# Kernel optimization log

Hardware: AMD Instinct MI355X
Metric: run time of the kernel (lower is better)

## Reference

```python
import jax, jax.numpy as jnp
import numpy as np

B, T, D, V, CD, NF = 2, 2048, 1024, 32000, 1024, 4
EPS_NORM = 1e-12
EPS_LN = 1e-5


def _gelu(x):
    return jax.nn.gelu(x, approximate=False)


def _l2norm(x):
    n = jnp.linalg.norm(x, axis=-1, keepdims=True)
    return x / jnp.maximum(n, EPS_NORM)


def setup_inputs() -> dict:
    key = jax.random.key(0)
    ks = jax.random.split(key, 24)
    s = 0.02
    inp = {
        "tokens": jax.random.randint(ks[0], (B, T), 0, V),
        "c_states": jax.random.normal(ks[1], (8, CD), dtype=jnp.float32),
        "embed": jax.random.normal(ks[2], (V, D), dtype=jnp.float32) * s,
        "pos_embed": jax.random.normal(ks[3], (T, D), dtype=jnp.float32) * s,
        # c_to_topo: Linear(c_dim,64) -> GELU -> Linear(64,2) -> Softplus (dead code in fwd, kept for completeness)
        "topo_W1": jax.random.normal(ks[4], (CD, 64), dtype=jnp.float32) * s,
        "topo_b1": jnp.zeros((64,), jnp.float32),
        "topo_W2": jax.random.normal(ks[5], (64, 2), dtype=jnp.float32) * s,
        "topo_b2": jnp.zeros((2,), jnp.float32),
        # c_to_thresh: Linear(c_dim,32) -> GELU -> Linear(32,NF) -> Sigmoid
        "thr_W1": jax.random.normal(ks[6], (CD, 32), dtype=jnp.float32) * s,
        "thr_b1": jnp.zeros((32,), jnp.float32),
        "thr_W2": jax.random.normal(ks[7], (32, NF), dtype=jnp.float32) * s,
        "thr_b2": jnp.zeros((NF,), jnp.float32),
        # simplex layers: NF x (Linear(2D,D) -> GELU -> Linear(D,D))
        "simp_W1": jax.random.normal(ks[8], (NF, 2 * D, D), dtype=jnp.float32) * s,
        "simp_b1": jnp.zeros((NF, D), jnp.float32),
        "simp_W2": jax.random.normal(ks[9], (NF, D, D), dtype=jnp.float32) * s,
        "simp_b2": jnp.zeros((NF, D), jnp.float32),
        # topo_integrate: Linear(D+2, 2D) -> GELU -> Linear(2D, D)
        "int_W1": jax.random.normal(ks[10], (D + 2, 2 * D), dtype=jnp.float32) * s,
        "int_b1": jnp.zeros((2 * D,), jnp.float32),
        "int_W2": jax.random.normal(ks[11], (2 * D, D), dtype=jnp.float32) * s,
        "int_b2": jnp.zeros((D,), jnp.float32),
        "ln_g": jnp.ones((D,), jnp.float32),
        "ln_b": jnp.zeros((D,), jnp.float32),
        "head_W": jax.random.normal(ks[12], (D, V), dtype=jnp.float32) * s,
    }
    return inp


def _forward(tokens, c_states, embed, pos_embed,
             topo_W1, topo_b1, topo_W2, topo_b2,
             thr_W1, thr_b1, thr_W2, thr_b2,
             simp_W1, simp_b1, simp_W2, simp_b2,
             int_W1, int_b1, int_W2, int_b2,
             ln_g, ln_b, head_W):
    b, t = tokens.shape
    x = embed[tokens] + pos_embed[jnp.arange(t)][None]          # [B,T,D]
    c_pooled = c_states.mean(axis=0)                            # [CD]
    thresholds = jax.nn.sigmoid(_gelu(c_pooled @ thr_W1 + thr_b1) @ thr_W2 + thr_b2)  # [NF]

    for level in range(NF):
        thresh = thresholds[level]
        x0 = x[0]                                               # [T,D] (module only uses batch elem 0)
        xn = _l2norm(x0)
        sim = xn @ xn.T                                         # [T,T]
        adj = jax.nn.sigmoid(10.0 * (sim - thresh))
        agg = adj @ x0                                          # dense message aggregation
        combined = jnp.concatenate([x0, agg], axis=-1)          # [T,2D]
        update = _gelu(combined @ simp_W1[level] + simp_b1[level]) @ simp_W2[level] + simp_b2[level]
        x = x + update[None] * 0.2                              # broadcast update across batch

    # approximate Betti numbers on detached embeddings
    xd = jax.lax.stop_gradient(x[0])
    xn = _l2norm(xd)
    sim = xn @ xn.T
    adj = jax.nn.sigmoid(10.0 * (sim - 0.5))
    degree = adj.sum(axis=-1)
    beta0 = (degree < 0.5).astype(jnp.float32).sum()
    n_edges = adj.sum() / 2.0
    beta1 = jax.nn.relu(n_edges - jnp.float32(t) + beta0 + 1.0)
    betti = jnp.stack([beta0, beta1])                           # [2]
    betti_exp = jnp.broadcast_to(betti[None, None, :], (b, t, 2))

    x = jnp.concatenate([x, betti_exp], axis=-1)                # [B,T,D+2]
    x = _gelu(x @ int_W1 + int_b1) @ int_W2 + int_b2            # [B,T,D]
    mu = x.mean(axis=-1, keepdims=True)
    var = x.var(axis=-1, keepdims=True)
    x = (x - mu) / jnp.sqrt(var + EPS_LN) * ln_g + ln_b
    return x @ head_W                                           # [B,T,V]


def reference(tokens, c_states, embed, pos_embed,
              topo_W1, topo_b1, topo_W2, topo_b2,
              thr_W1, thr_b1, thr_W2, thr_b2,
              simp_W1, simp_b1, simp_W2, simp_b2,
              int_W1, int_b1, int_W2, int_b2,
              ln_g, ln_b, head_W):
    return _forward(tokens, c_states, embed, pos_embed,
                    topo_W1, topo_b1, topo_W2, topo_b2,
                    thr_W1, thr_b1, thr_W2, thr_b2,
                    simp_W1, simp_b1, simp_W2, simp_b2,
                    int_W1, int_b1, int_W2, int_b2,
                    ln_g, ln_b, head_W)
```

## Files before the change

### kernel.cpp

```cpp
#include <hip/hip_runtime.h>

typedef __bf16 bf16;
using bf16x8 = __attribute__((ext_vector_type(8))) __bf16;
using bf16x4 = __attribute__((ext_vector_type(4))) __bf16;
using f32x4  = __attribute__((ext_vector_type(4))) float;

#define DEV __device__ __forceinline__
#define SCHED_FENCE() __builtin_amdgcn_sched_barrier(0)

DEV float gelu_f(float x){ return 0.5f*x*(1.0f+erff(x*0.7071067811865475f)); }
DEV float sigm_f(float x){ return 1.0f/(1.0f+expf(-x)); }

DEV void gload16(const bf16* g, bf16* l){
    __builtin_amdgcn_global_load_lds(
        (const __attribute__((address_space(1))) void*)g,
        (__attribute__((address_space(3))) void*)l, 16, 0, 0);
}

enum { EPI_ADJ=0, EPI_BF16=1, EPI_GELU_BIAS=2, EPI_XUPD=3, EPI_BIAS_F32=4, EPI_F32=5,
       EPI_XUPDB=6, EPI_XUPDT=7 };

template<int BM,int BN,int WM,int WN,int MINW,int EPI>
__global__ __launch_bounds__(WM*WN*64, MINW)
void gemm_p(const bf16* __restrict__ A, const bf16* __restrict__ B,
            int M, int N, int K, void* __restrict__ Cout, int ldc,
            const float* __restrict__ bias, const float* __restrict__ scal, int sidx,
            float* __restrict__ xu0, float* __restrict__ xu1, bf16* __restrict__ xbp)
{
    constexpr int THREADS = WM*WN*64;
    constexpr int MR = BM/WM/16, NR = BN/WN/16;
    constexpr int ATILE = BM*64, BTILE = BN*64;
    constexpr int RR = THREADS/8;
    constexpr int VM = (BM+BN)/RR;
    __shared__ bf16 sm[2*(ATILE+BTILE)];

    const int nbm = M/BM, nbn = N/BN;
    const int nwg = nbm*nbn;
    int wg = blockIdx.x;
    wg = (wg&7)*(nwg>>3) + (wg>>3);
    const int by = wg % nbm, bx = wg / nbm;
    const int tid = threadIdx.x, lane = tid&63, wid = tid>>6;
    const int wm = wid / WN, wn = wid % WN;
    const int fr = lane&15, fq = lane>>4;

    const bf16* Ab = A + (long)(by*BM + (tid>>3))*K + (((tid&7) ^ ((tid>>3)&7))<<3);
    const bf16* Bb = B + (long)(bx*BN + (tid>>3))*K + (((tid&7) ^ ((tid>>3)&7))<<3);

    auto STAGE = [&](int tt, int cb){
        bf16* d = sm + cb*(ATILE+BTILE) + wid*512;
        const long ko = (long)tt*64;
#pragma unroll
        for (int g=0; g<BM/RR; ++g)
            gload16(Ab + (long)g*RR*K + ko, d + g*RR*64);
#pragma unroll
        for (int g=0; g<BN/RR; ++g)
            gload16(Bb + (long)g*RR*K + ko, d + ATILE + g*RR*64);
    };

    f32x4 acc[MR][NR] = {};
    const int nt = K >> 6;

    STAGE(0,0);
    STAGE(1,1);

    for (int t=0; t<nt; ++t){
        const bf16* bufA = sm + (t&1)*(ATILE+BTILE);
        const bf16* bufB = bufA + ATILE;
        if (t+1<nt){
            if constexpr (VM==4)      asm volatile("s_waitcnt vmcnt(4)" ::: "memory");
            else if constexpr (VM==6) asm volatile("s_waitcnt vmcnt(6)" ::: "memory");
            else if constexpr (VM==8) asm volatile("s_waitcnt vmcnt(8)" ::: "memory");
            else                      asm volatile("s_waitcnt vmcnt(0)" ::: "memory");
        } else {
            asm volatile("s_waitcnt vmcnt(0)" ::: "memory");
        }
        __builtin_amdgcn_s_barrier();
        __builtin_amdgcn_sched_barrier(0);
#pragma unroll
        for (int ks=0; ks<2; ++ks){
            bf16x8 af[MR], bv[NR];
            const int ch = (((ks*4+fq) ^ (fr&7))<<3);
#pragma unroll
            for (int j=0;j<MR;++j)
                af[j] = *(const bf16x8*)&bufA[(wm*(MR*16) + j*16 + fr)*64 + ch];
#pragma unroll
            for (int j=0;j<NR;++j)
                bv[j] = *(const bf16x8*)&bufB[(wn*(NR*16) + j*16 + fr)*64 + ch];
            __builtin_amdgcn_s_setprio(1);
#pragma unroll
            for (int mi=0;mi<MR;++mi)
#pragma unroll
            for (int ni=0;ni<NR;++ni)
                acc[mi][ni] = __builtin_amdgcn_mfma_f32_16x16x32_bf16(
                    af[mi], bv[ni], acc[mi][ni], 0,0,0);
            __builtin_amdgcn_s_setprio(0);
        }
        asm volatile("s_waitcnt lgkmcnt(0)" ::: "memory");
        __builtin_amdgcn_s_barrier();
        if (t+2<nt) STAGE(t+2, t&1);
    }

    float thr = 0.f;
    if constexpr (EPI==EPI_ADJ) thr = scal[sidx];

#pragma unroll
    for (int mi=0;mi<MR;++mi){
#pragma unroll
        for (int ni=0;ni<NR;++ni){
            const int col = bx*BN + wn*(NR*16) + ni*16 + fr;
#pragma unroll
            for (int r=0;r<4;++r){
                const int row = by*BM + wm*(MR*16) + mi*16 + fq*4 + r;
                const float v = acc[mi][ni][r];
                const long ci = (long)row*ldc + col;
                if constexpr (EPI==EPI_ADJ)       ((bf16*)Cout)[ci] = (bf16)sigm_f(10.f*(v - thr));
                else if constexpr (EPI==EPI_BF16) ((bf16*)Cout)[ci] = (bf16)v;
                else if constexpr (EPI==EPI_GELU_BIAS) ((bf16*)Cout)[ci] = (bf16)gelu_f(v + bias[col]);
                else if constexpr (EPI==EPI_BIAS_F32)  ((float*)Cout)[ci] = v + bias[col];
                else if constexpr (EPI==EPI_F32)       ((float*)Cout)[ci] = v;
                else if constexpr (EPI==EPI_XUPD){
                    const float u = 0.2f*(v + bias[col]);
                    xu0[ci] += u;  xu1[ci] += u;
                }
                else if constexpr (EPI==EPI_XUPDB){
                    const float u = 0.2f*(v + bias[col]);
                    const float n0 = xu0[ci] + u, n1 = xu1[ci] + u;
                    xu0[ci] = n0;  xu1[ci] = n1;
                    xbp[ci] = (bf16)n0;
                    xbp[ci + (long)2048*1024] = (bf16)n1;
                }
                else if constexpr (EPI==EPI_XUPDT){
                    const float u = 0.2f*(v + bias[col]);
                    const float n0 = xu0[ci] + u, n1 = xu1[ci] + u;
                    xu0[ci] = n0;  xu1[ci] = n1;
                    ((bf16*)Cout)[(long)row*2048 + col] = (bf16)n0;
                    xbp[(long)col*2048 + row] = (bf16)n0;
                }
            }
        }
    }
}

template<int EPI>
__global__ __launch_bounds__(512, 2)
void gemm8(const bf16* __restrict__ A, const bf16* __restrict__ B,
           int M, int N, int K, void* __restrict__ Cout, int ldc,
           const float* __restrict__ bias)
{
    __shared__ bf16 sm[65536];
    const int nbm = M>>8;
    const int wg = blockIdx.x;
    const int by = wg % nbm, bx = wg / nbm;
    const int tid = threadIdx.x, lane = tid&63, wid = tid>>6;
    const int wm = wid>>2, wn = wid&3;
    const int fr = lane&15, fq = lane>>4;

    const bf16* Ag = A + (long)(by*256 + (tid>>3))*K + (((tid&7) ^ ((tid>>3)&7))<<3);
    const bf16* Bg = B + (long)(bx*256 + (tid>>3))*K + (((tid&7) ^ ((tid>>3)&7))<<3);

    auto SA = [&](int tt, int h){
        bf16* d = sm + (tt&1)*32768 + wid*512;
        const long ko = (long)tt*64;
        gload16(Ag + (long)(h*64)*K + ko,       d + h*4096);
        gload16(Ag + (long)(128+h*64)*K + ko,   d + 8192 + h*4096);
    };
    auto SB = [&](int tt, int h){
        bf16* d = sm + (tt&1)*32768 + 16384 + wid*512;
        const long ko = (long)tt*64;
#pragma unroll
        for (int g=0; g<2; ++g)
            gload16(Bg + (long)(h*2+g)*64*K + ko, d + (h*2+g)*4096);
    };

    f32x4 acc[8][4] = {};
    bf16x8 aCur[8], b0[4], b1[4];
    const int nt = K >> 6;

    SA(0,0); SB(0,0); SA(0,1); SB(0,1);
    SA(1,0); SB(1,0); SA(1,1);
    SCHED_FENCE();

    for (int t=0; t<nt; ++t){
        const bf16* bufA = sm + (t&1)*32768;
        const bf16* bufB = bufA + 16384;

        auto LDA = [&](int mh){
#pragma unroll
            for (int ks=0;ks<2;++ks){
                const int ch = (((ks*4+fq) ^ (fr&7))<<3);
#pragma unroll
                for (int j=0;j<4;++j)
                    aCur[ks*4+j] = *(const bf16x8*)&bufA[(wm*128 + mh*64 + j*16 + fr)*64 + ch];
            }
        };
        auto LDB = [&](int nh, bf16x8* dst){
#pragma unroll
            for (int ks=0;ks<2;++ks){
                const int ch = (((ks*4+fq) ^ (fr&7))<<3);
#pragma unroll
                for (int j=0;j<2;++j)
                    dst[ks*2+j] = *(const bf16x8*)&bufB[(wn*64 + nh*32 + j*16 + fr)*64 + ch];
            }
        };
        auto QMFMA = [&](int mh, int nh, bf16x8* bArr){
            __builtin_amdgcn_s_setprio(1);
#pragma unroll
            for (int ks=0;ks<2;++ks)
#pragma unroll
            for (int j=0;j<4;++j)
#pragma unroll
            for (int jj=0;jj<2;++jj)
                acc[mh*4+j][nh*2+jj] = __builtin_amdgcn_mfma_f32_16x16x32_bf16(
                    aCur[ks*4+j], bArr[ks*2+jj], acc[mh*4+j][nh*2+jj], 0,0,0);
            __builtin_amdgcn_s_setprio(0);
            SCHED_FENCE();
        };

        if (t+1<nt) asm volatile("s_waitcnt vmcnt(6)" ::: "memory");
        else        asm volatile("s_waitcnt vmcnt(0)" ::: "memory");
        __builtin_amdgcn_s_barrier();
        SCHED_FENCE();
        if (t+1<nt) SB(t+1,1);
        SCHED_FENCE();
        LDA(0); LDB(0, b0);
        asm volatile("s_waitcnt lgkmcnt(0)" ::: "memory");
        SCHED_FENCE();
        QMFMA(0,0,b0);
        __builtin_amdgcn_s_barrier();
        SCHED_FENCE();
        if (t+2<nt) SA(t+2,0);
        SCHED_FENCE();
        LDB(1, b1);
        asm volatile("s_waitcnt lgkmcnt(0)" ::: "memory");
        SCHED_FENCE();
        QMFMA(0,1,b1);
        __builtin_amdgcn_s_barrier();
        SCHED_FENCE();
        if (t+2<nt) SB(t+2,0);
        SCHED_FENCE();
        LDA(1);
        asm volatile("s_waitcnt lgkmcnt(0)" ::: "memory");
        SCHED_FENCE();
        QMFMA(1,1,b1);
        __builtin_amdgcn_s_barrier();
        SCHED_FENCE();
        if (t+2<nt) SA(t+2,1);
        SCHED_FENCE();
        QMFMA(1,0,b0);
    }

#pragma unroll
    for (int mi=0;mi<8;++mi){
#pragma unroll
        for (int ni=0;ni<4;++ni){
            const int col = bx*256 + wn*64 + ni*16 + fr;
#pragma unroll
            for (int r=0;r<4;++r){
                const int row = by*256 + wm*128 + mi*16 + fq*4 + r;
                const float v = acc[mi][ni][r];
                const long ci = (long)row*ldc + col;
                if constexpr (EPI==EPI_F32)            ((float*)Cout)[ci] = v;
                else if constexpr (EPI==EPI_BIAS_F32)  ((float*)Cout)[ci] = v + bias[col];
                else                                   ((bf16*)Cout)[ci] = (bf16)v;
            }
        }
    }
}

__global__ void prep_kernel(const float* __restrict__ cs,
                            const float* __restrict__ W1, const float* __restrict__ b1,
                            const float* __restrict__ W2, const float* __restrict__ b2,
                            float* __restrict__ thrs)
{
    __shared__ float cp[1024];
    __shared__ float part[8][32];
    __shared__ float h[32];
    const int tid = threadIdx.x;
    for (int j = tid; j < 1024; j += 256){
        float s = 0.f;
#pragma unroll
        for (int r = 0; r < 8; r++) s += cs[r*1024 + j];
        cp[j] = s * 0.125f;
    }
    __syncthreads();
    const int t = tid & 31, g = tid >> 5;
    float p = 0.f;
    for (int j = g*128; j < g*128+128; j++) p += cp[j] * W1[j*32 + t];
    part[g][t] = p;
    __syncthreads();
    if (tid < 32){
        float s = b1[tid];
#pragma unroll
        for (int q=0;q<8;q++) s += part[q][tid];
        h[tid] = gelu_f(s);
    }
    __syncthreads();
    if (tid < 4){
        float z = b2[tid];
        for (int k=0;k<32;k++) z += h[k]*W2[k*4 + tid];
        thrs[tid] = sigm_f(z);
    }
    if (tid == 4) thrs[4] = 0.5f;
}

__global__ void embed_kernel(const int* __restrict__ tok, const float* __restrict__ emb,
                             const float* __restrict__ pos, float* __restrict__ x)
{
    const long i = (long)blockIdx.x*256 + threadIdx.x;
    const int  d4 = i & 255;
    const long bt = i >> 8;
    const int  t  = (int)(bt & 2047);
    const int  token = tok[bt];
    f32x4 e = *(const f32x4*)(emb + (long)token*1024 + d4*4);
    f32x4 p = *(const f32x4*)(pos + (long)t*1024 + d4*4);
    *(f32x4*)(x + i*4) = e + p;
}

__global__ void transpose_f2b(const float* __restrict__ in, int ldin, long istr,
                              bf16* __restrict__ out, int ldout, long ostr,
                              int R, int C)
{
    __shared__ float tile[32][33];
    const int nbx = C >> 5, nby = R >> 5;
    const int per = nbx*nby;
    const int l  = blockIdx.x / per;
    const int rm = blockIdx.x % per;
    const int bx = rm % nbx, by = rm / nbx;
    const float* inl = in + (long)l*istr;
    bf16* outl = out + (long)l*ostr;
    const int tx = threadIdx.x & 31, ty = threadIdx.x >> 5;
#pragma unroll
    for (int i=0;i<32;i+=8)
        tile[ty+i][tx] = inl[(long)(by*32+ty+i)*ldin + bx*32+tx];
    __syncthreads();
#pragma unroll
    for (int i=0;i<32;i+=8)
        outl[(long)(bx*32+ty+i)*ldout + by*32+tx] = (bf16)tile[tx][ty+i];
}

__global__ void rownorm_kernel(const float* __restrict__ x, bf16* __restrict__ xn,
                               bf16* __restrict__ x0b, int ld0)
{
    const long t = blockIdx.x; const int tid = threadIdx.x;
    f32x4 v = *(const f32x4*)(x + t*1024 + tid*4);
    float s = v.x*v.x + v.y*v.y + v.z*v.z + v.w*v.w;
#pragma unroll
    for (int o=32;o>0;o>>=1) s += __shfl_down(s, o);
    __shared__ float red[4];
    if ((tid&63)==0) red[tid>>6] = s;
    __syncthreads();
    const float tot = red[0]+red[1]+red[2]+red[3];
    const float inv = 1.0f / fmaxf(sqrtf(tot), 1e-12f);
    bf16x4 a;
    a[0]=(bf16)(v.x*inv); a[1]=(bf16)(v.y*inv); a[2]=(bf16)(v.z*inv); a[3]=(bf16)(v.w*inv);
    *(bf16x4*)(xn + t*1024 + tid*4) = a;
    if (x0b){
        bf16x4 b;
        b[0]=(bf16)v.x; b[1]=(bf16)v.y; b[2]=(bf16)v.z; b[3]=(bf16)v.w;
        *(bf16x4*)(x0b + t*ld0 + tid*4) = b;
    }
}

__global__ void degree_kernel(const bf16* __restrict__ adj, float* __restrict__ deg)
{
    const long t = blockIdx.x; const int tid = threadIdx.x;
    bf16x8 v = *(const bf16x8*)(adj + t*2048 + tid*8);
    float s = 0.f;
#pragma unroll
    for (int j=0;j<8;j++) s += (float)v[j];
#pragma unroll
    for (int o=32;o>0;o>>=1) s += __shfl_down(s, o);
    __shared__ float red[4];
    if ((tid&63)==0) red[tid>>6] = s;
    __syncthreads();
    if (tid==0) deg[t] = red[0]+red[1]+red[2]+red[3];
}

__global__ void betti_kernel(const float* __restrict__ deg, float* __restrict__ betti)
{
    const int tid = threadIdx.x;
    float s = 0.f, c = 0.f;
#pragma unroll
    for (int i=0;i<8;i++){
        const float d = deg[tid*8 + i];
        s += d;  c += (d < 0.5f) ? 1.f : 0.f;
    }
#pragma unroll
    for (int o=32;o>0;o>>=1){ s += __shfl_down(s,o); c += __shfl_down(c,o); }
    __shared__ float ss[4], cc[4];
    if ((tid&63)==0){ ss[tid>>6]=s; cc[tid>>6]=c; }
    __syncthreads();
    if (tid==0){
        const float S = ss[0]+ss[1]+ss[2]+ss[3];
        const float C = cc[0]+cc[1]+cc[2]+cc[3];
        const float ne = 0.5f*S;
        const float b1 = ne - 2048.f + C + 1.f;
        betti[0] = C;
        betti[1] = b1 > 0.f ? b1 : 0.f;
    }
}

__global__ void b1eff_kernel(const float* __restrict__ ib1, const float* __restrict__ iW1,
                             const float* __restrict__ betti, float* __restrict__ out)
{
    const int j = blockIdx.x*256 + threadIdx.x;
    out[j] = ib1[j] + betti[0]*iW1[(long)1024*2048 + j] + betti[1]*iW1[(long)1025*2048 + j];
}

__global__ void ln_kernel(const float* __restrict__ y, const float* __restrict__ g,
                          const float* __restrict__ b, bf16* __restrict__ out)
{
    const long t = blockIdx.x; const int tid = threadIdx.x;
    f32x4 v = *(const f32x4*)(y + t*1024 + tid*4);
    float s  = v.x+v.y+v.z+v.w;
    float s2 = v.x*v.x+v.y*v.y+v.z*v.z+v.w*v.w;
#pragma unroll
    for (int o=32;o>0;o>>=1){ s += __shfl_down(s,o); s2 += __shfl_down(s2,o); }
    __shared__ float ss[4], qq[4];
    if ((tid&63)==0){ ss[tid>>6]=s; qq[tid>>6]=s2; }
    __syncthreads();
    const float S = ss[0]+ss[1]+ss[2]+ss[3], Q = qq[0]+qq[1]+qq[2]+qq[3];
    const float mu  = S * (1.f/1024.f);
    const float var = Q * (1.f/1024.f) - mu*mu;
    const float inv = rsqrtf(var + 1e-5f);
    f32x4 gv = *(const f32x4*)(g + tid*4);
    f32x4 bv = *(const f32x4*)(b + tid*4);
    bf16x4 o;
    o[0] = (bf16)((v.x - mu)*inv*gv.x + bv.x);
    o[1] = (bf16)((v.y - mu)*inv*gv.y + bv.y);
    o[2] = (bf16)((v.z - mu)*inv*gv.z + bv.z);
    o[3] = (bf16)((v.w - mu)*inv*gv.w + bv.w);
    *(bf16x4*)(out + t*1024 + tid*4) = o;
}

extern "C" void kernel_launch(void* const* d_in, const int* in_sizes, int n_in,
                              void* d_out, int out_size, void* d_ws, size_t ws_size,
                              hipStream_t stream)
{
    const int*   tokens = (const int*)  d_in[0];
    const float* cstate = (const float*)d_in[1];
    const float* embedW = (const float*)d_in[2];
    const float* posW   = (const float*)d_in[3];
    const float* thrW1  = (const float*)d_in[8];
    const float* thrb1  = (const float*)d_in[9];
    const float* thrW2  = (const float*)d_in[10];
    const float* thrb2  = (const float*)d_in[11];
    const float* simpW1 = (const float*)d_in[12];
    const float* simpb1 = (const float*)d_in[13];
    const float* simpW2 = (const float*)d_in[14];
    const float* simpb2 = (const float*)d_in[15];
    const float* intW1  = (const float*)d_in[16];
    const float* intb1  = (const float*)d_in[17];
    const float* intW2  = (const float*)d_in[18];
    const float* intb2  = (const float*)d_in[19];
    const float* lng    = (const float*)d_in[20];
    const float* lnb    = (const float*)d_in[21];
    const float* headW  = (const float*)d_in[22];
    float* out = (float*)d_out;

    size_t off = 0;
    auto carve = [&](size_t bytes) -> void* {
        void* p = (char*)d_ws + off;
        off += (bytes + 255) & ~(size_t)255;
        return p;
    };
    float* x_f32   = (float*)carve(16777216);
    bf16*  xn      = (bf16*) carve(4194304);
    bf16*  x0T     = (bf16*) carve(4194304);
    bf16*  comb    = (bf16*) carve(8388608);
    bf16*  adj     = (bf16*) carve(8388608);
    bf16*  h1      = (bf16*) carve(4194304);
    bf16*  xb      = (bf16*) carve(8388608);
    bf16*  w1T     = (bf16*) carve(16777216);
    bf16*  w2T     = (bf16*) carve(8388608);
    bf16*  i1T     = (bf16*) carve(4194304);
    bf16*  i2T     = (bf16*) carve(4194304);
    bf16*  hT      = (bf16*) carve(65536000);
    float* degree  = (float*)carve(8192);
    float* b1eff   = (float*)carve(8192);
    float* thrs    = (float*)carve(64);
    float* betti   = (float*)carve(64);
    bf16*  h2  = comb;
    float* yv  = x_f32;
    bf16*  xln = xn;

    const dim3 blk(256);
    const dim3 blk512(512);

    prep_kernel<<<1, blk, 0, stream>>>(cstate, thrW1, thrb1, thrW2, thrb2, thrs);
    embed_kernel<<<4096, blk, 0, stream>>>(tokens, embedW, posW, x_f32);

    transpose_f2b<<<4*(1024/32)*(2048/32), blk, 0, stream>>>(
        simpW1, 1024, (long)2048*1024, w1T, 2048, (long)1024*2048, 2048, 1024);
    transpose_f2b<<<4*(1024/32)*(1024/32), blk, 0, stream>>>(
        simpW2, 1024, (long)1024*1024, w2T, 1024, (long)1024*1024, 1024, 1024);
    transpose_f2b<<<(2048/32)*(1024/32), blk, 0, stream>>>(
        intW1, 2048, 0, i1T, 1024, 0, 1024, 2048);
    transpose_f2b<<<(1024/32)*(2048/32), blk, 0, stream>>>(
        intW2, 1024, 0, i2T, 2048, 0, 2048, 1024);
    transpose_f2b<<<(32000/32)*(1024/32), blk, 0, stream>>>(
        headW, 32000, 0, hT, 1024, 0, 1024, 32000);

    for (int l=0;l<4;l++){
        if (l == 0){
            rownorm_kernel<<<2048, blk, 0, stream>>>(x_f32, xn, comb, 2048);
            transpose_f2b<<<(1024/32)*(2048/32), blk, 0, stream>>>(
                x_f32, 1024, 0, x0T, 2048, 0, 2048, 1024);
        } else {
            rownorm_kernel<<<2048, blk, 0, stream>>>(x_f32, xn, nullptr, 0);
        }
        gemm_p<64,128,2,2,3,EPI_ADJ><<<32*16, blk, 0, stream>>>(
            xn, xn, 2048, 2048, 1024, adj, 2048, nullptr, thrs, l, nullptr, nullptr, nullptr);
        gemm_p<64,64,2,2,4,EPI_BF16><<<32*16, blk, 0, stream>>>(
            adj, x0T, 2048, 1024, 2048, comb + 1024, 2048, nullptr, nullptr, 0, nullptr, nullptr, nullptr);
        gemm_p<64,64,2,2,4,EPI_GELU_BIAS><<<32*16, blk, 0, stream>>>(
            comb, w1T + (long)l*1024*2048, 2048, 1024, 2048, h1, 1024,
            simpb1 + l*1024, nullptr, 0, nullptr, nullptr, nullptr);
        if (l < 3)
            gemm_p<64,64,2,2,4,EPI_XUPDT><<<32*16, blk, 0, stream>>>(
                h1, w2T + (long)l*1024*1024, 2048, 1024, 1024, comb, 1024,
                simpb2 + l*1024, nullptr, 0, x_f32, x_f32 + (long)2048*1024, x0T);
        else
            gemm_p<64,64,2,2,4,EPI_XUPDB><<<32*16, blk, 0, stream>>>(
                h1, w2T + (long)l*1024*1024, 2048, 1024, 1024, nullptr, 1024,
                simpb2 + l*1024, nullptr, 0, x_f32, x_f32 + (long)2048*1024, xb);
    }

    rownorm_kernel<<<2048, blk, 0, stream>>>(x_f32, xn, nullptr, 0);
    gemm_p<64,128,2,2,3,EPI_ADJ><<<32*16, blk, 0, stream>>>(
        xn, xn, 2048, 2048, 1024, adj, 2048, nullptr, thrs, 4, nullptr, nullptr, nullptr);
    degree_kernel<<<2048, blk, 0, stream>>>(adj, degree);
    betti_kernel<<<1, blk, 0, stream>>>(degree, betti);
    b1eff_kernel<<<8, blk, 0, stream>>>(intb1, intW1, betti, b1eff);

    gemm_p<128,128,2,2,2,EPI_GELU_BIAS><<<32*16, blk, 0, stream>>>(
        xb, i1T, 4096, 2048, 1024, h2, 2048, b1eff, nullptr, 0, nullptr, nullptr, nullptr);
    gemm_p<64,128,2,2,3,EPI_BIAS_F32><<<64*8, blk, 0, stream>>>(
        h2, i2T, 4096, 1024, 2048, yv, 1024, intb2, nullptr, 0, nullptr, nullptr, nullptr);
    ln_kernel<<<4096, blk, 0, stream>>>(yv, lng, lnb, xln);
    gemm8<EPI_F32><<<16*125, blk512, 0, stream>>>(
        xln, hT, 4096, 32000, 1024, out, 32000, nullptr);
}
```

Before: 802.6 us.

## Fuse degree reduction into final adjacency GEMM and store batch delta instead of duplicate state

The final adjacency GEMM now reduces its sigmoid outputs per row and atomically adds them into a degree vector. This removes the write of the full bf16 adjacency matrix and the separate degree kernel, at the cost of an extra zeroing launch and atomics. The second batch's state is also stored as a fixed difference from the first, since both receive identical updates, so the simplex-layer epilogues update only one fp32 array and rebuild the second when writing the final bf16 copy. This relies on the update being identical across batches and changes fp32 rounding slightly.

```diff
diff --git a/kernel.cpp b/kernel.cpp
--- a/kernel.cpp
+++ b/kernel.cpp
@@ -18,7 +18,7 @@
 }
 
 enum { EPI_ADJ=0, EPI_BF16=1, EPI_GELU_BIAS=2, EPI_XUPD=3, EPI_BIAS_F32=4, EPI_F32=5,
-       EPI_XUPDB=6, EPI_XUPDT=7 };
+       EPI_XUPDB=6, EPI_XUPDT=7, EPI_DEG=8 };
 
 template<int BM,int BN,int WM,int WN,int MINW,int EPI>
 __global__ __launch_bounds__(WM*WN*64, MINW)
@@ -101,7 +101,28 @@
     }
 
     float thr = 0.f;
-    if constexpr (EPI==EPI_ADJ) thr = scal[sidx];
+    if constexpr (EPI==EPI_ADJ || EPI==EPI_DEG) thr = scal[sidx];
+
+    if constexpr (EPI==EPI_DEG){
+        float* deg = (float*)Cout;
+#pragma unroll
+        for (int mi=0;mi<MR;++mi){
+#pragma unroll
+            for (int r=0;r<4;++r){
+                float s = 0.f;
+#pragma unroll
+                for (int ni=0;ni<NR;++ni)
+                    s += sigm_f(10.f*(acc[mi][ni][r] - thr));
+                s += __shfl_xor(s, 1);
+                s += __shfl_xor(s, 2);
+                s += __shfl_xor(s, 4);
+                s += __shfl_xor(s, 8);
+                if (fr == 0)
+                    atomicAdd(&deg[by*BM + wm*(MR*16) + mi*16 + fq*4 + r], s);
+            }
+        }
+        return;
+    }
 
 #pragma unroll
     for (int mi=0;mi<MR;++mi){
@@ -120,19 +141,19 @@
                 else if constexpr (EPI==EPI_F32)       ((float*)Cout)[ci] = v;
                 else if constexpr (EPI==EPI_XUPD){
                     const float u = 0.2f*(v + bias[col]);
-                    xu0[ci] += u;  xu1[ci] += u;
+                    xu0[ci] += u;
                 }
                 else if constexpr (EPI==EPI_XUPDB){
                     const float u = 0.2f*(v + bias[col]);
-                    const float n0 = xu0[ci] + u, n1 = xu1[ci] + u;
-                    xu0[ci] = n0;  xu1[ci] = n1;
+                    const float n0 = xu0[ci] + u;
+                    xu0[ci] = n0;
                     xbp[ci] = (bf16)n0;
-                    xbp[ci + (long)2048*1024] = (bf16)n1;
+                    xbp[ci + (long)2048*1024] = (bf16)(n0 + xu1[ci]);
                 }
                 else if constexpr (EPI==EPI_XUPDT){
                     const float u = 0.2f*(v + bias[col]);
-                    const float n0 = xu0[ci] + u, n1 = xu1[ci] + u;
-                    xu0[ci] = n0;  xu1[ci] = n1;
+                    const float n0 = xu0[ci] + u;
+                    xu0[ci] = n0;
                     ((bf16*)Cout)[(long)row*2048 + col] = (bf16)n0;
                     xbp[(long)col*2048 + row] = (bf16)n0;
                 }
@@ -310,10 +331,14 @@
     const int  d4 = i & 255;
     const long bt = i >> 8;
     const int  t  = (int)(bt & 2047);
-    const int  token = tok[bt];
-    f32x4 e = *(const f32x4*)(emb + (long)token*1024 + d4*4);
-    f32x4 p = *(const f32x4*)(pos + (long)t*1024 + d4*4);
-    *(f32x4*)(x + i*4) = e + p;
+    f32x4 e1 = *(const f32x4*)(emb + (long)tok[bt]*1024 + d4*4);
+    if (bt < 2048){
+        f32x4 p = *(const f32x4*)(pos + (long)t*1024 + d4*4);
+        *(f32x4*)(x + i*4) = e1 + p;
+    } else {
+        f32x4 e0 = *(const f32x4*)(emb + (long)tok[t]*1024 + d4*4);
+        *(f32x4*)(x + i*4) = e1 - e0;
+    }
 }
 
 __global__ void transpose_f2b(const float* __restrict__ in, int ldin, long istr,
@@ -361,19 +386,9 @@
     }
 }
 
-__global__ void degree_kernel(const bf16* __restrict__ adj, float* __restrict__ deg)
-{
-    const long t = blockIdx.x; const int tid = threadIdx.x;
-    bf16x8 v = *(const bf16x8*)(adj + t*2048 + tid*8);
-    float s = 0.f;
-#pragma unroll
-    for (int j=0;j<8;j++) s += (float)v[j];
-#pragma unroll
-    for (int o=32;o>0;o>>=1) s += __shfl_down(s, o);
-    __shared__ float red[4];
-    if ((tid&63)==0) red[tid>>6] = s;
-    __syncthreads();
-    if (tid==0) deg[t] = red[0]+red[1]+red[2]+red[3];
+__global__ void zero_kernel(float* __restrict__ p)
+{
+    p[blockIdx.x*256 + threadIdx.x] = 0.f;
 }
 
 __global__ void betti_kernel(const float* __restrict__ deg, float* __restrict__ betti)
@@ -519,7 +534,7 @@
         if (l < 3)
             gemm_p<64,64,2,2,4,EPI_XUPDT><<<32*16, blk, 0, stream>>>(
                 h1, w2T + (long)l*1024*1024, 2048, 1024, 1024, comb, 1024,
-                simpb2 + l*1024, nullptr, 0, x_f32, x_f32 + (long)2048*1024, x0T);
+                simpb2 + l*1024, nullptr, 0, x_f32, nullptr, x0T);
         else
             gemm_p<64,64,2,2,4,EPI_XUPDB><<<32*16, blk, 0, stream>>>(
                 h1, w2T + (long)l*1024*1024, 2048, 1024, 1024, nullptr, 1024,
@@ -527,9 +542,9 @@
     }
 
     rownorm_kernel<<<2048, blk, 0, stream>>>(x_f32, xn, nullptr, 0);
-    gemm_p<64,128,2,2,3,EPI_ADJ><<<32*16, blk, 0, stream>>>(
-        xn, xn, 2048, 2048, 1024, adj, 2048, nullptr, thrs, 4, nullptr, nullptr, nullptr);
-    degree_kernel<<<2048, blk, 0, stream>>>(adj, degree);
+    zero_kernel<<<8, blk, 0, stream>>>(degree);
+    gemm_p<64,128,2,2,3,EPI_DEG><<<32*16, blk, 0, stream>>>(
+        xn, xn, 2048, 2048, 1024, degree, 0, nullptr, thrs, 4, nullptr, nullptr, nullptr);
     betti_kernel<<<1, blk, 0, stream>>>(degree, betti);
     b1eff_kernel<<<8, blk, 0, stream>>>(intb1, intW1, betti, b1eff);
 
```

Measured after the change: 796.4 us. No clear change (-0.8%).
